# Kernel optimization log

Hardware: AMD Instinct MI355X
Metric: run time of the kernel (lower is better)

The kernel has to match this reference:

```python
import jax, jax.numpy as jnp
import numpy as np

B, H, P, L = 8, 512, 512, 2048
HIGH_STAB, LOW_STAB = 0.9, 0.99  # 0 <= high < |lambda| <= low <= 1 (discrete dynamics)


def setup_inputs() -> dict:
    key = jax.random.key(0)
    k_u, k_mag, k_ph, k_b, k_c, k_d = jax.random.split(key, 6)
    u = jax.random.normal(k_u, (B, H, L), dtype=jnp.float32)
    # Frozen diagonal reservoir state matrix Lambda_bar: complex eigenvalues with
    # magnitude in (high_stability, low_stability], random phase (stored as real/imag pairs).
    mag = jax.random.uniform(k_mag, (P,), minval=HIGH_STAB, maxval=LOW_STAB)
    phase = jax.random.uniform(k_ph, (P,), minval=0.0, maxval=2.0 * np.pi)
    Lambda_bar_ri = jnp.stack([mag * jnp.cos(phase), mag * jnp.sin(phase)], axis=-1)  # (P,2)
    B_bar_ri = jax.random.normal(k_b, (P, H, 2), dtype=jnp.float32)  # complex B_bar as real pairs
    C_ri = jax.random.normal(k_c, (H, P, 2), dtype=jnp.float32)      # complex C as real pairs
    D = jax.random.normal(k_d, (H, H), dtype=jnp.float32)
    return {"u": u, "Lambda_bar_ri": Lambda_bar_ri, "B_bar_ri": B_bar_ri, "C_ri": C_ri, "D": D}


def _binary_op(e_i, e_j):
    A_i, Bu_i = e_i
    A_j, Bu_j = e_j
    return (A_j * A_i, A_j * Bu_i + Bu_j)


def reference(u, Lambda_bar_ri, B_bar_ri, C_ri, D):
    Lam = jax.lax.complex(Lambda_bar_ri[:, 0], Lambda_bar_ri[:, 1])        # (P,)
    B_bar = jax.lax.complex(B_bar_ri[..., 0], B_bar_ri[..., 1])            # (P,H)
    C = jax.lax.complex(C_ri[..., 0], C_ri[..., 1])                        # (H,P)
    # Bu_t = B_bar @ u_t for all t, batched: (B,P,L) complex
    Bu = jnp.einsum('ph,bhl->bpl', B_bar, u.astype(B_bar.dtype))
    A = jnp.broadcast_to(Lam[None, :, None], Bu.shape)                     # (B,P,L)
    # Parallel associative scan: x_t = Lam * x_{t-1} + Bu_t
    _, x = jax.lax.associative_scan(_binary_op, (A, Bu), axis=2)           # (B,P,L)
    C_A_Bu = jnp.einsum('hp,bpl->bhl', C, x).real                          # (B,H,L)
    # torch.einsum('hh,bhl->bhl', D, u) uses only the diagonal of D
    Du = jnp.diagonal(D)[None, :, None] * u
    return jax.nn.gelu(C_A_Bu + Du, approximate=False)
```

## Files before the change

kernel.cpp:

```cpp
#include <hip/hip_runtime.h>
#include <cstdint>
#include <cstddef>

#define BB 8
#define HH 512
#define PP 512
#define LL 2048

typedef __attribute__((ext_vector_type(8))) __bf16 bf16x8;
typedef __attribute__((ext_vector_type(4))) float f32x4;

__device__ __forceinline__ uint16_t f2bf(float f) {
  uint32_t u = __builtin_bit_cast(uint32_t, f);
  u += 0x7FFFu + ((u >> 16) & 1u);
  return (uint16_t)(u >> 16);
}

__device__ __forceinline__ void async_copy16(const void* gptr, void* ldsptr) {
  __builtin_amdgcn_global_load_lds(
      (const __attribute__((address_space(1))) unsigned int*)gptr,
      (__attribute__((address_space(3))) unsigned int*)ldsptr,
      16, 0, 0);
}

__global__ __launch_bounds__(256) void prep_mats(
    const float* __restrict__ Bbar, const float* __restrict__ Cri,
    const float* __restrict__ Dm,
    uint16_t* __restrict__ A1, uint16_t* __restrict__ A2,
    float* __restrict__ Dd) {
  int idx = blockIdx.x * 256 + threadIdx.x;
  int p = idx >> 9, h = idx & 511;
  A1[(size_t)p * 512 + h]          = f2bf(Bbar[((size_t)p * 512 + h) * 2 + 0]);
  A1[(size_t)(512 + p) * 512 + h]  = f2bf(Bbar[((size_t)p * 512 + h) * 2 + 1]);
  int h2 = idx >> 9, p2 = idx & 511;
  A2[(size_t)h2 * 1024 + p2]        = f2bf( Cri[((size_t)h2 * 512 + p2) * 2 + 0]);
  A2[(size_t)h2 * 1024 + 512 + p2]  = f2bf(-Cri[((size_t)h2 * 512 + p2) * 2 + 1]);
  if (idx < 512) Dd[idx] = Dm[(size_t)idx * 512 + idx];
}

__global__ __launch_bounds__(256) void scan_kernel(
    const float* __restrict__ Lam, uint16_t* __restrict__ Bu) {
  const int gt = blockIdx.x * 256 + threadIdx.x;
  const int wave = gt >> 6, lane = gt & 63;
  const int b = wave >> 9, p = wave & 511;
  const float lr = Lam[p * 2 + 0], li = Lam[p * 2 + 1];
  float ar = lr, ai = li;
#pragma unroll
  for (int s = 0; s < 5; ++s) { float nr = ar * ar - ai * ai, ni = 2.f * ar * ai; ar = nr; ai = ni; }

  uint16_t* rowre = Bu + ((size_t)(b * 1024 + p)) * 2048 + lane * 32;
  uint16_t* rowim = Bu + ((size_t)(b * 1024 + 512 + p)) * 2048 + lane * 32;
  uint4 vr[4], vi[4];
#pragma unroll
  for (int q = 0; q < 4; ++q) { vr[q] = ((const uint4*)rowre)[q]; vi[q] = ((const uint4*)rowim)[q]; }

  float xr[32], xi[32];
  float sr = 0.f, si = 0.f;
#pragma unroll
  for (int q = 0; q < 4; ++q) {
    uint32_t wr[4] = {vr[q].x, vr[q].y, vr[q].z, vr[q].w};
    uint32_t wi[4] = {vi[q].x, vi[q].y, vi[q].z, vi[q].w};
#pragma unroll
    for (int d = 0; d < 4; ++d) {
      float br0 = __builtin_bit_cast(float, wr[d] << 16);
      float bi0 = __builtin_bit_cast(float, wi[d] << 16);
      float br1 = __builtin_bit_cast(float, wr[d] & 0xFFFF0000u);
      float bi1 = __builtin_bit_cast(float, wi[d] & 0xFFFF0000u);
      int j = q * 8 + d * 2;
      float nr = lr * sr - li * si + br0, ni = lr * si + li * sr + bi0;
      sr = nr; si = ni; xr[j] = sr; xi[j] = si;
      nr = lr * sr - li * si + br1; ni = lr * si + li * sr + bi1;
      sr = nr; si = ni; xr[j + 1] = sr; xi[j + 1] = si;
    }
  }
  float Ar = ar, Ai = ai, Sr = sr, Si = si;
#pragma unroll
  for (int off = 1; off < 64; off <<= 1) {
    float pAr = __shfl_up(Ar, off), pAi = __shfl_up(Ai, off);
    float pSr = __shfl_up(Sr, off), pSi = __shfl_up(Si, off);
    if (lane >= off) {
      float tSr = Ar * pSr - Ai * pSi + Sr;
      float tSi = Ar * pSi + Ai * pSr + Si;
      float tAr = Ar * pAr - Ai * pAi;
      float tAi = Ar * pAi + Ai * pAr;
      Sr = tSr; Si = tSi; Ar = tAr; Ai = tAi;
    }
  }
  float Cr = __shfl_up(Sr, 1), Ci = __shfl_up(Si, 1);
  if (lane == 0) { Cr = 0.f; Ci = 0.f; }
  float fr_ = lr * Cr - li * Ci, fi_ = lr * Ci + li * Cr;
#pragma unroll
  for (int j = 0; j < 32; ++j) {
    xr[j] += fr_; xi[j] += fi_;
    float nfr = fr_ * lr - fi_ * li, nfi = fr_ * li + fi_ * lr;
    fr_ = nfr; fi_ = nfi;
  }
#pragma unroll
  for (int q = 0; q < 4; ++q) {
    uint32_t wr[4], wi[4];
#pragma unroll
    for (int d = 0; d < 4; ++d) {
      int j = q * 8 + d * 2;
      wr[d] = (uint32_t)f2bf(xr[j]) | ((uint32_t)f2bf(xr[j + 1]) << 16);
      wi[d] = (uint32_t)f2bf(xi[j]) | ((uint32_t)f2bf(xi[j + 1]) << 16);
    }
    ((uint4*)rowre)[q] = make_uint4(wr[0], wr[1], wr[2], wr[3]);
    ((uint4*)rowim)[q] = make_uint4(wi[0], wi[1], wi[2], wi[3]);
  }
}

__global__ __launch_bounds__(256) void gemm1_fused(
    const uint16_t* __restrict__ A, const float* __restrict__ U,
    uint16_t* __restrict__ Bu) {
  __shared__ __align__(16) uint16_t Alds[2][128 * 32];
  __shared__ __align__(16) uint16_t Blds[2][128 * 40];
  const int t = threadIdx.x, lane = t & 63, w = t >> 6;
  const int m0 = blockIdx.y * 128, n0 = blockIdx.x * 128, b = blockIdx.z;

  const int ra = t >> 2;
  const int qa = ((t & 3) ^ ((ra >> 1) & 3)) * 8;
  const uint16_t* gA0 = A + (size_t)(m0 + ra) * 512 + qa;
  const uint16_t* gA1 = A + (size_t)(m0 + 64 + ra) * 512 + qa;

  const int kp = t >> 4, lg = t & 15;
  const float* gB = U + ((size_t)b * 512 + 2 * kp) * 2048 + n0 + lg * 8;
  const int bcol = ((kp >> 2) ^ (lg & 3)) * 8 + (kp & 3) * 2;

  f32x4 acc[4][4];
#pragma unroll
  for (int i = 0; i < 4; ++i)
#pragma unroll
    for (int j = 0; j < 4; ++j) acc[i][j] = (f32x4){0.f, 0.f, 0.f, 0.f};

  const int wm = (w >> 1) * 64, wn = (w & 1) * 64;
  const int fr = lane & 15, fq = lane >> 4;
  const int aswz = (fq ^ ((fr >> 1) & 3)) * 8;

  float4 pb0, pb1, pb2, pb3;
  async_copy16(gA0, &Alds[0][t * 8]);
  async_copy16(gA1, &Alds[0][2048 + t * 8]);
  pb0 = *(const float4*)(gB);
  pb1 = *(const float4*)(gB + 4);
  pb2 = *(const float4*)(gB + 2048);
  pb3 = *(const float4*)(gB + 2052);
  {
    float r0[8] = {pb0.x, pb0.y, pb0.z, pb0.w, pb1.x, pb1.y, pb1.z, pb1.w};
    float r1[8] = {pb2.x, pb2.y, pb2.z, pb2.w, pb3.x, pb3.y, pb3.z, pb3.w};
#pragma unroll
    for (int j = 0; j < 8; ++j)
      *(uint32_t*)&Blds[0][(lg * 8 + j) * 40 + bcol] =
          (uint32_t)f2bf(r0[j]) | ((uint32_t)f2bf(r1[j]) << 16);
  }
  __syncthreads();

#pragma unroll 2
  for (int it = 0; it < 16; ++it) {
    const int cur = it & 1, nxt = cur ^ 1;
    const bool pre = (it < 15);
    if (pre) {
      const int kb = (it + 1) * 32;
      async_copy16(gA0 + kb, &Alds[nxt][t * 8]);
      async_copy16(gA1 + kb, &Alds[nxt][2048 + t * 8]);
      const float* s0 = gB + (size_t)kb * 2048;
      pb0 = *(const float4*)(s0);
      pb1 = *(const float4*)(s0 + 4);
      pb2 = *(const float4*)(s0 + 2048);
      pb3 = *(const float4*)(s0 + 2052);
    }
    bf16x8 af[4], bfr[4];
#pragma unroll
    for (int i = 0; i < 4; ++i)
      af[i] = *(const bf16x8*)&Alds[cur][(wm + i * 16 + fr) * 32 + aswz];
#pragma unroll
    for (int j = 0; j < 4; ++j) {
      int n = wn + j * 16 + fr;
      bfr[j] = *(const bf16x8*)&Blds[cur][n * 40 + ((fq ^ ((n >> 3) & 3)) * 8)];
    }
#pragma unroll
    for (int i = 0; i < 4; ++i)
#pragma unroll
      for (int j = 0; j < 4; ++j)
        acc[i][j] = __builtin_amdgcn_mfma_f32_16x16x32_bf16(af[i], bfr[j], acc[i][j], 0, 0, 0);
    if (pre) {
      float r0[8] = {pb0.x, pb0.y, pb0.z, pb0.w, pb1.x, pb1.y, pb1.z, pb1.w};
      float r1[8] = {pb2.x, pb2.y, pb2.z, pb2.w, pb3.x, pb3.y, pb3.z, pb3.w};
#pragma unroll
      for (int j = 0; j < 8; ++j)
        *(uint32_t*)&Blds[nxt][(lg * 8 + j) * 40 + bcol] =
            (uint32_t)f2bf(r0[j]) | ((uint32_t)f2bf(r1[j]) << 16);
      __syncthreads();
    }
  }

  uint16_t* O = Bu + ((size_t)b * 1024 + m0) * 2048 + n0;
#pragma unroll
  for (int i = 0; i < 4; ++i)
#pragma unroll
    for (int j = 0; j < 4; ++j)
#pragma unroll
      for (int r = 0; r < 4; ++r) {
        int mm = wm + i * 16 + fq * 4 + r;
        int nn = wn + j * 16 + fr;
        O[(size_t)mm * 2048 + nn] = f2bf(acc[i][j][r]);
      }
}

__global__ __launch_bounds__(256) void gemm2_fused(
    const uint16_t* __restrict__ A, const uint16_t* __restrict__ X,
    float* __restrict__ Out, const float* __restrict__ Dd,
    const float* __restrict__ Uu) {
  __shared__ __align__(16) uint16_t Alds[2][128 * 32];
  __shared__ __align__(16) uint16_t Blds[2][128 * 40];
  const int t = threadIdx.x, lane = t & 63, w = t >> 6;
  const int m0 = blockIdx.y * 128, n0 = blockIdx.x * 128, b = blockIdx.z;

  const int ra = t >> 2;
  const int qa = ((t & 3) ^ ((ra >> 1) & 3)) * 8;
  const uint16_t* gA0 = A + (size_t)(m0 + ra) * 1024 + qa;
  const uint16_t* gA1 = A + (size_t)(m0 + 64 + ra) * 1024 + qa;

  const int kp = t >> 4, lg = t & 15;
  const uint16_t* gB = X + ((size_t)b * 1024 + 2 * kp) * 2048 + n0 + lg * 8;
  const int bcol = ((kp >> 2) ^ (lg & 3)) * 8 + (kp & 3) * 2;

  f32x4 acc[4][4];
#pragma unroll
  for (int i = 0; i < 4; ++i)
#pragma unroll
    for (int j = 0; j < 4; ++j) acc[i][j] = (f32x4){0.f, 0.f, 0.f, 0.f};

  const int wm = (w >> 1) * 64, wn = (w & 1) * 64;
  const int fr = lane & 15, fq = lane >> 4;
  const int aswz = (fq ^ ((fr >> 1) & 3)) * 8;

  uint4 q0, q1;
  async_copy16(gA0, &Alds[0][t * 8]);
  async_copy16(gA1, &Alds[0][2048 + t * 8]);
  q0 = *(const uint4*)(gB);
  q1 = *(const uint4*)(gB + 2048);
  {
    uint32_t u0[4] = {q0.x, q0.y, q0.z, q0.w};
    uint32_t u1[4] = {q1.x, q1.y, q1.z, q1.w};
#pragma unroll
    for (int d = 0; d < 4; ++d) {
      *(uint32_t*)&Blds[0][(lg * 8 + 2 * d + 0) * 40 + bcol] = (u0[d] & 0xFFFFu) | (u1[d] << 16);
      *(uint32_t*)&Blds[0][(lg * 8 + 2 * d + 1) * 40 + bcol] = (u0[d] >> 16) | (u1[d] & 0xFFFF0000u);
    }
  }
  __syncthreads();

#pragma unroll 2
  for (int it = 0; it < 32; ++it) {
    const int cur = it & 1, nxt = cur ^ 1;
    const bool pre = (it < 31);
    if (pre) {
      const int kb = (it + 1) * 32;
      async_copy16(gA0 + kb, &Alds[nxt][t * 8]);
      async_copy16(gA1 + kb, &Alds[nxt][2048 + t * 8]);
      const uint16_t* s0 = gB + (size_t)kb * 2048;
      q0 = *(const uint4*)(s0);
      q1 = *(const uint4*)(s0 + 2048);
    }
    bf16x8 af[4], bfr[4];
#pragma unroll
    for (int i = 0; i < 4; ++i)
      af[i] = *(const bf16x8*)&Alds[cur][(wm + i * 16 + fr) * 32 + aswz];
#pragma unroll
    for (int j = 0; j < 4; ++j) {
      int n = wn + j * 16 + fr;
      bfr[j] = *(const bf16x8*)&Blds[cur][n * 40 + ((fq ^ ((n >> 3) & 3)) * 8)];
    }
#pragma unroll
    for (int i = 0; i < 4; ++i)
#pragma unroll
      for (int j = 0; j < 4; ++j)
        acc[i][j] = __builtin_amdgcn_mfma_f32_16x16x32_bf16(af[i], bfr[j], acc[i][j], 0, 0, 0);
    if (pre) {
      uint32_t u0[4] = {q0.x, q0.y, q0.z, q0.w};
      uint32_t u1[4] = {q1.x, q1.y, q1.z, q1.w};
#pragma unroll
      for (int d = 0; d < 4; ++d) {
        *(uint32_t*)&Blds[nxt][(lg * 8 + 2 * d + 0) * 40 + bcol] = (u0[d] & 0xFFFFu) | (u1[d] << 16);
        *(uint32_t*)&Blds[nxt][(lg * 8 + 2 * d + 1) * 40 + bcol] = (u0[d] >> 16) | (u1[d] & 0xFFFF0000u);
      }
      __syncthreads();
    }
  }

  const size_t base = ((size_t)b * 512 + m0) * 2048 + n0;
  float* O = Out + base;
  const float* Ub = Uu + base;
#pragma unroll
  for (int i = 0; i < 4; ++i)
#pragma unroll
    for (int r = 0; r < 4; ++r) {
      int mm = wm + i * 16 + fq * 4 + r;
      float dv = Dd[m0 + mm];
#pragma unroll
      for (int j = 0; j < 4; ++j) {
        int nn = wn + j * 16 + fr;
        float xv = acc[i][j][r] + dv * Ub[(size_t)mm * 2048 + nn];
        O[(size_t)mm * 2048 + nn] = 0.5f * xv * (1.f + erff(xv * 0.70710678118654752f));
      }
    }
}

extern "C" void kernel_launch(void* const* d_in, const int* in_sizes, int n_in,
                              void* d_out, int out_size, void* d_ws, size_t ws_size,
                              hipStream_t stream) {
  const float* u    = (const float*)d_in[0];
  const float* Lam  = (const float*)d_in[1];
  const float* Bbar = (const float*)d_in[2];
  const float* Cri  = (const float*)d_in[3];
  const float* Dm   = (const float*)d_in[4];
  float* out = (float*)d_out;

  char* ws = (char*)d_ws;
  uint16_t* Bu = (uint16_t*)(ws);
  uint16_t* A1 = (uint16_t*)(ws + 33554432);
  uint16_t* A2 = (uint16_t*)(ws + 34603008);
  float*    Dd = (float*)   (ws + 35651584);

  prep_mats<<<1024, 256, 0, stream>>>(Bbar, Cri, Dm, A1, A2, Dd);
  gemm1_fused<<<dim3(16, 8, BB), 256, 0, stream>>>(A1, u, Bu);
  scan_kernel<<<1024, 256, 0, stream>>>(Lam, Bu);
  gemm2_fused<<<dim3(16, 4, BB), 256, 0, stream>>>(A2, Bu, out, Dd, u);
}
```

Before: 196.3 us.

## Pre-transpose GEMM B operands so both GEMMs load B via async LDS copies

Adds a transpose of u to bf16 in L-major layout, fused into the prep kernel, and a separate transpose kernel for the scanned state X. Both GEMMs can then stream their B tiles with global_load_lds async copies in the same swizzled K-contiguous layout as A. This removes the per-iteration register round trip, bf16 conversion and scattered LDS stores for B. In exchange it adds an extra kernel launch and a full read and write pass over the 32 MB X buffer, plus a transposed copy of u, and it doubles workspace usage.

```diff
diff --git a/kernel.cpp b/kernel.cpp
--- a/kernel.cpp
+++ b/kernel.cpp
@@ -23,19 +23,44 @@
       16, 0, 0);
 }
 
-__global__ __launch_bounds__(256) void prep_mats(
-    const float* __restrict__ Bbar, const float* __restrict__ Cri,
-    const float* __restrict__ Dm,
-    uint16_t* __restrict__ A1, uint16_t* __restrict__ A2,
-    float* __restrict__ Dd) {
-  int idx = blockIdx.x * 256 + threadIdx.x;
-  int p = idx >> 9, h = idx & 511;
-  A1[(size_t)p * 512 + h]          = f2bf(Bbar[((size_t)p * 512 + h) * 2 + 0]);
-  A1[(size_t)(512 + p) * 512 + h]  = f2bf(Bbar[((size_t)p * 512 + h) * 2 + 1]);
-  int h2 = idx >> 9, p2 = idx & 511;
-  A2[(size_t)h2 * 1024 + p2]        = f2bf( Cri[((size_t)h2 * 512 + p2) * 2 + 0]);
-  A2[(size_t)h2 * 1024 + 512 + p2]  = f2bf(-Cri[((size_t)h2 * 512 + p2) * 2 + 1]);
-  if (idx < 512) Dd[idx] = Dm[(size_t)idx * 512 + idx];
+__global__ __launch_bounds__(256) void prep_and_transpose(
+    const float* __restrict__ U, const float* __restrict__ Bbar,
+    const float* __restrict__ Cri, const float* __restrict__ Dm,
+    uint16_t* __restrict__ Ut, uint16_t* __restrict__ A1,
+    uint16_t* __restrict__ A2, float* __restrict__ Dd) {
+  __shared__ uint16_t tile[64][66];
+  const int t = threadIdx.x;
+  if (blockIdx.x < 2048) {
+    const int bid = blockIdx.x;
+    const int b = bid >> 8;
+    const int h0 = ((bid >> 5) & 7) * 64;
+    const int l0 = (bid & 31) * 64;
+    const int r = t >> 2, c = t & 3;
+    const float* src = U + ((size_t)(b * 512 + h0 + r)) * 2048 + l0 + c * 16;
+#pragma unroll
+    for (int q = 0; q < 4; ++q) {
+      float4 v = *(const float4*)(src + q * 4);
+      *(uint32_t*)&tile[r][c * 16 + q * 4]     = (uint32_t)f2bf(v.x) | ((uint32_t)f2bf(v.y) << 16);
+      *(uint32_t*)&tile[r][c * 16 + q * 4 + 2] = (uint32_t)f2bf(v.z) | ((uint32_t)f2bf(v.w) << 16);
+    }
+    __syncthreads();
+    uint16_t* dst = Ut + ((size_t)(b * 2048 + l0 + r)) * 512 + h0 + c * 16;
+    uint32_t o[8];
+#pragma unroll
+    for (int k = 0; k < 8; ++k)
+      o[k] = (uint32_t)tile[c * 16 + 2 * k][r] | ((uint32_t)tile[c * 16 + 2 * k + 1][r] << 16);
+    *(uint4*)(dst)     = make_uint4(o[0], o[1], o[2], o[3]);
+    *(uint4*)(dst + 8) = make_uint4(o[4], o[5], o[6], o[7]);
+  } else {
+    int idx = (blockIdx.x - 2048) * 256 + t;
+    int p = idx >> 9, h = idx & 511;
+    A1[(size_t)p * 512 + h]          = f2bf(Bbar[((size_t)p * 512 + h) * 2 + 0]);
+    A1[(size_t)(512 + p) * 512 + h]  = f2bf(Bbar[((size_t)p * 512 + h) * 2 + 1]);
+    int h2 = idx >> 9, p2 = idx & 511;
+    A2[(size_t)h2 * 1024 + p2]        = f2bf( Cri[((size_t)h2 * 512 + p2) * 2 + 0]);
+    A2[(size_t)h2 * 1024 + 512 + p2]  = f2bf(-Cri[((size_t)h2 * 512 + p2) * 2 + 1]);
+    if (idx < 512) Dd[idx] = Dm[(size_t)idx * 512 + idx];
+  }
 }
 
 __global__ __launch_bounds__(256) void scan_kernel(
@@ -109,22 +134,47 @@
   }
 }
 
+__global__ __launch_bounds__(256) void transpose_x(
+    const uint16_t* __restrict__ X, uint16_t* __restrict__ Xt) {
+  __shared__ uint16_t tile[64][66];
+  const int t = threadIdx.x;
+  const int b = blockIdx.z, p0 = blockIdx.y * 64, l0 = blockIdx.x * 64;
+  const int r = t >> 2, c = t & 3;
+  const uint16_t* src = X + ((size_t)(b * 1024 + p0 + r)) * 2048 + l0 + c * 16;
+  uint4 v0 = *(const uint4*)(src);
+  uint4 v1 = *(const uint4*)(src + 8);
+  *(uint32_t*)&tile[r][c * 16 + 0]  = v0.x;
+  *(uint32_t*)&tile[r][c * 16 + 2]  = v0.y;
+  *(uint32_t*)&tile[r][c * 16 + 4]  = v0.z;
+  *(uint32_t*)&tile[r][c * 16 + 6]  = v0.w;
+  *(uint32_t*)&tile[r][c * 16 + 8]  = v1.x;
+  *(uint32_t*)&tile[r][c * 16 + 10] = v1.y;
+  *(uint32_t*)&tile[r][c * 16 + 12] = v1.z;
+  *(uint32_t*)&tile[r][c * 16 + 14] = v1.w;
+  __syncthreads();
+  uint16_t* dst = Xt + ((size_t)(b * 2048 + l0 + r)) * 1024 + p0 + c * 16;
+  uint32_t o[8];
+#pragma unroll
+  for (int k = 0; k < 8; ++k)
+    o[k] = (uint32_t)tile[c * 16 + 2 * k][r] | ((uint32_t)tile[c * 16 + 2 * k + 1][r] << 16);
+  *(uint4*)(dst)     = make_uint4(o[0], o[1], o[2], o[3]);
+  *(uint4*)(dst + 8) = make_uint4(o[4], o[5], o[6], o[7]);
+}
+
 __global__ __launch_bounds__(256) void gemm1_fused(
-    const uint16_t* __restrict__ A, const float* __restrict__ U,
+    const uint16_t* __restrict__ A, const uint16_t* __restrict__ Bt,
     uint16_t* __restrict__ Bu) {
   __shared__ __align__(16) uint16_t Alds[2][128 * 32];
-  __shared__ __align__(16) uint16_t Blds[2][128 * 40];
+  __shared__ __align__(16) uint16_t Blds[2][128 * 32];
   const int t = threadIdx.x, lane = t & 63, w = t >> 6;
   const int m0 = blockIdx.y * 128, n0 = blockIdx.x * 128, b = blockIdx.z;
 
   const int ra = t >> 2;
   const int qa = ((t & 3) ^ ((ra >> 1) & 3)) * 8;
   const uint16_t* gA0 = A + (size_t)(m0 + ra) * 512 + qa;
-  const uint16_t* gA1 = A + (size_t)(m0 + 64 + ra) * 512 + qa;
-
-  const int kp = t >> 4, lg = t & 15;
-  const float* gB = U + ((size_t)b * 512 + 2 * kp) * 2048 + n0 + lg * 8;
-  const int bcol = ((kp >> 2) ^ (lg & 3)) * 8 + (kp & 3) * 2;
+  const uint16_t* gA1 = gA0 + (size_t)64 * 512;
+  const uint16_t* gB0 = Bt + ((size_t)b * 2048 + n0 + ra) * 512 + qa;
+  const uint16_t* gB1 = gB0 + (size_t)64 * 512;
 
   f32x4 acc[4][4];
 #pragma unroll
@@ -134,23 +184,12 @@
 
   const int wm = (w >> 1) * 64, wn = (w & 1) * 64;
   const int fr = lane & 15, fq = lane >> 4;
-  const int aswz = (fq ^ ((fr >> 1) & 3)) * 8;
-
-  float4 pb0, pb1, pb2, pb3;
+  const int swz = (fq ^ ((fr >> 1) & 3)) * 8;
+
   async_copy16(gA0, &Alds[0][t * 8]);
   async_copy16(gA1, &Alds[0][2048 + t * 8]);
-  pb0 = *(const float4*)(gB);
-  pb1 = *(const float4*)(gB + 4);
-  pb2 = *(const float4*)(gB + 2048);
-  pb3 = *(const float4*)(gB + 2052);
-  {
-    float r0[8] = {pb0.x, pb0.y, pb0.z, pb0.w, pb1.x, pb1.y, pb1.z, pb1.w};
-    float r1[8] = {pb2.x, pb2.y, pb2.z, pb2.w, pb3.x, pb3.y, pb3.z, pb3.w};
-#pragma unroll
-    for (int j = 0; j < 8; ++j)
-      *(uint32_t*)&Blds[0][(lg * 8 + j) * 40 + bcol] =
-          (uint32_t)f2bf(r0[j]) | ((uint32_t)f2bf(r1[j]) << 16);
-  }
+  async_copy16(gB0, &Blds[0][t * 8]);
+  async_copy16(gB1, &Blds[0][2048 + t * 8]);
   __syncthreads();
 
 #pragma unroll 2
@@ -161,35 +200,22 @@
       const int kb = (it + 1) * 32;
       async_copy16(gA0 + kb, &Alds[nxt][t * 8]);
       async_copy16(gA1 + kb, &Alds[nxt][2048 + t * 8]);
-      const float* s0 = gB + (size_t)kb * 2048;
-      pb0 = *(const float4*)(s0);
-      pb1 = *(const float4*)(s0 + 4);
-      pb2 = *(const float4*)(s0 + 2048);
-      pb3 = *(const float4*)(s0 + 2052);
+      async_copy16(gB0 + kb, &Blds[nxt][t * 8]);
+      async_copy16(gB1 + kb, &Blds[nxt][2048 + t * 8]);
     }
     bf16x8 af[4], bfr[4];
 #pragma unroll
     for (int i = 0; i < 4; ++i)
-      af[i] = *(const bf16x8*)&Alds[cur][(wm + i * 16 + fr) * 32 + aswz];
-#pragma unroll
-    for (int j = 0; j < 4; ++j) {
-      int n = wn + j * 16 + fr;
-      bfr[j] = *(const bf16x8*)&Blds[cur][n * 40 + ((fq ^ ((n >> 3) & 3)) * 8)];
-    }
+      af[i] = *(const bf16x8*)&Alds[cur][(wm + i * 16 + fr) * 32 + swz];
+#pragma unroll
+    for (int j = 0; j < 4; ++j)
+      bfr[j] = *(const bf16x8*)&Blds[cur][(wn + j * 16 + fr) * 32 + swz];
 #pragma unroll
     for (int i = 0; i < 4; ++i)
 #pragma unroll
       for (int j = 0; j < 4; ++j)
         acc[i][j] = __builtin_amdgcn_mfma_f32_16x16x32_bf16(af[i], bfr[j], acc[i][j], 0, 0, 0);
-    if (pre) {
-      float r0[8] = {pb0.x, pb0.y, pb0.z, pb0.w, pb1.x, pb1.y, pb1.z, pb1.w};
-      float r1[8] = {pb2.x, pb2.y, pb2.z, pb2.w, pb3.x, pb3.y, pb3.z, pb3.w};
-#pragma unroll
-      for (int j = 0; j < 8; ++j)
-        *(uint32_t*)&Blds[nxt][(lg * 8 + j) * 40 + bcol] =
-            (uint32_t)f2bf(r0[j]) | ((uint32_t)f2bf(r1[j]) << 16);
-      __syncthreads();
-    }
+    if (pre) __syncthreads();
   }
 
   uint16_t* O = Bu + ((size_t)b * 1024 + m0) * 2048 + n0;
@@ -206,22 +232,20 @@
 }
 
 __global__ __launch_bounds__(256) void gemm2_fused(
-    const uint16_t* __restrict__ A, const uint16_t* __restrict__ X,
+    const uint16_t* __restrict__ A, const uint16_t* __restrict__ Bt,
     float* __restrict__ Out, const float* __restrict__ Dd,
     const float* __restrict__ Uu) {
   __shared__ __align__(16) uint16_t Alds[2][128 * 32];
-  __shared__ __align__(16) uint16_t Blds[2][128 * 40];
+  __shared__ __align__(16) uint16_t Blds[2][128 * 32];
   const int t = threadIdx.x, lane = t & 63, w = t >> 6;
   const int m0 = blockIdx.y * 128, n0 = blockIdx.x * 128, b = blockIdx.z;
 
   const int ra = t >> 2;
   const int qa = ((t & 3) ^ ((ra >> 1) & 3)) * 8;
   const uint16_t* gA0 = A + (size_t)(m0 + ra) * 1024 + qa;
-  const uint16_t* gA1 = A + (size_t)(m0 + 64 + ra) * 1024 + qa;
-
-  const int kp = t >> 4, lg = t & 15;
-  const uint16_t* gB = X + ((size_t)b * 1024 + 2 * kp) * 2048 + n0 + lg * 8;
-  const int bcol = ((kp >> 2) ^ (lg & 3)) * 8 + (kp & 3) * 2;
+  const uint16_t* gA1 = gA0 + (size_t)64 * 1024;
+  const uint16_t* gB0 = Bt + ((size_t)b * 2048 + n0 + ra) * 1024 + qa;
+  const uint16_t* gB1 = gB0 + (size_t)64 * 1024;
 
   f32x4 acc[4][4];
 #pragma unroll
@@ -231,22 +255,12 @@
 
   const int wm = (w >> 1) * 64, wn = (w & 1) * 64;
   const int fr = lane & 15, fq = lane >> 4;
-  const int aswz = (fq ^ ((fr >> 1) & 3)) * 8;
-
-  uint4 q0, q1;
+  const int swz = (fq ^ ((fr >> 1) & 3)) * 8;
+
   async_copy16(gA0, &Alds[0][t * 8]);
   async_copy16(gA1, &Alds[0][2048 + t * 8]);
-  q0 = *(const uint4*)(gB);
-  q1 = *(const uint4*)(gB + 2048);
-  {
-    uint32_t u0[4] = {q0.x, q0.y, q0.z, q0.w};
-    uint32_t u1[4] = {q1.x, q1.y, q1.z, q1.w};
-#pragma unroll
-    for (int d = 0; d < 4; ++d) {
-      *(uint32_t*)&Blds[0][(lg * 8 + 2 * d + 0) * 40 + bcol] = (u0[d] & 0xFFFFu) | (u1[d] << 16);
-      *(uint32_t*)&Blds[0][(lg * 8 + 2 * d + 1) * 40 + bcol] = (u0[d] >> 16) | (u1[d] & 0xFFFF0000u);
-    }
-  }
+  async_copy16(gB0, &Blds[0][t * 8]);
+  async_copy16(gB1, &Blds[0][2048 + t * 8]);
   __syncthreads();
 
 #pragma unroll 2
@@ -257,34 +271,22 @@
       const int kb = (it + 1) * 32;
       async_copy16(gA0 + kb, &Alds[nxt][t * 8]);
       async_copy16(gA1 + kb, &Alds[nxt][2048 + t * 8]);
-      const uint16_t* s0 = gB + (size_t)kb * 2048;
-      q0 = *(const uint4*)(s0);
-      q1 = *(const uint4*)(s0 + 2048);
+      async_copy16(gB0 + kb, &Blds[nxt][t * 8]);
+      async_copy16(gB1 + kb, &Blds[nxt][2048 + t * 8]);
     }
     bf16x8 af[4], bfr[4];
 #pragma unroll
     for (int i = 0; i < 4; ++i)
-      af[i] = *(const bf16x8*)&Alds[cur][(wm + i * 16 + fr) * 32 + aswz];
-#pragma unroll
-    for (int j = 0; j < 4; ++j) {
-      int n = wn + j * 16 + fr;
-      bfr[j] = *(const bf16x8*)&Blds[cur][n * 40 + ((fq ^ ((n >> 3) & 3)) * 8)];
-    }
+      af[i] = *(const bf16x8*)&Alds[cur][(wm + i * 16 + fr) * 32 + swz];
+#pragma unroll
+    for (int j = 0; j < 4; ++j)
+      bfr[j] = *(const bf16x8*)&Blds[cur][(wn + j * 16 + fr) * 32 + swz];
 #pragma unroll
     for (int i = 0; i < 4; ++i)
 #pragma unroll
       for (int j = 0; j < 4; ++j)
         acc[i][j] = __builtin_amdgcn_mfma_f32_16x16x32_bf16(af[i], bfr[j], acc[i][j], 0, 0, 0);
-    if (pre) {
-      uint32_t u0[4] = {q0.x, q0.y, q0.z, q0.w};
-      uint32_t u1[4] = {q1.x, q1.y, q1.z, q1.w};
-#pragma unroll
-      for (int d = 0; d < 4; ++d) {
-        *(uint32_t*)&Blds[nxt][(lg * 8 + 2 * d + 0) * 40 + bcol] = (u0[d] & 0xFFFFu) | (u1[d] << 16);
-        *(uint32_t*)&Blds[nxt][(lg * 8 + 2 * d + 1) * 40 + bcol] = (u0[d] >> 16) | (u1[d] & 0xFFFF0000u);
-      }
-      __syncthreads();
-    }
+    if (pre) __syncthreads();
   }
 
   const size_t base = ((size_t)b * 512 + m0) * 2048 + n0;
@@ -317,12 +319,15 @@
 
   char* ws = (char*)d_ws;
   uint16_t* Bu = (uint16_t*)(ws);
-  uint16_t* A1 = (uint16_t*)(ws + 33554432);
-  uint16_t* A2 = (uint16_t*)(ws + 34603008);
-  float*    Dd = (float*)   (ws + 35651584);
-
-  prep_mats<<<1024, 256, 0, stream>>>(Bbar, Cri, Dm, A1, A2, Dd);
-  gemm1_fused<<<dim3(16, 8, BB), 256, 0, stream>>>(A1, u, Bu);
+  uint16_t* Xt = (uint16_t*)(ws + 33554432);
+  uint16_t* Ut = (uint16_t*)(ws + 33554432);
+  uint16_t* A1 = (uint16_t*)(ws + 67108864);
+  uint16_t* A2 = (uint16_t*)(ws + 68157440);
+  float*    Dd = (float*)   (ws + 69206016);
+
+  prep_and_transpose<<<3072, 256, 0, stream>>>(u, Bbar, Cri, Dm, Ut, A1, A2, Dd);
+  gemm1_fused<<<dim3(16, 8, BB), 256, 0, stream>>>(A1, Ut, Bu);
   scan_kernel<<<1024, 256, 0, stream>>>(Lam, Bu);
-  gemm2_fused<<<dim3(16, 4, BB), 256, 0, stream>>>(A2, Bu, out, Dd, u);
-}
+  transpose_x<<<dim3(32, 16, BB), 256, 0, stream>>>(Bu, Xt);
+  gemm2_fused<<<dim3(16, 4, BB), 256, 0, stream>>>(A2, Xt, out, Dd, u);
+}
```

Result: no change. 193.8 us (-1.3%).
